# Optimization experiments

Measured on AMD Instinct MI355X. Metric: run time of the kernel, lower is better.

## Reference

```python
import jax, jax.numpy as jnp
import numpy as np


def _maxpool(x, k):
    # NCHW max pool with window k, stride k, no padding
    return jax.lax.reduce_window(
        x, -jnp.inf, jax.lax.max,
        window_dimensions=(1, 1, k, k),
        window_strides=(1, 1, k, k),
        padding='VALID')


def setup_inputs() -> dict:
    key = jax.random.key(0)
    k1, k2, k3, k4, k5 = jax.random.split(key, 5)
    return {
        'input_tensor1': jax.random.normal(k1, (8, 128, 56, 56), dtype=jnp.float32),
        'input_tensor2': jax.random.normal(k2, (8, 64, 112, 112), dtype=jnp.float32),
        'input_tensor3': jax.random.normal(k3, (8, 32, 224, 224), dtype=jnp.float32),
        'input_tensor4': jax.random.normal(k4, (8, 16, 448, 448), dtype=jnp.float32),
        'pure_ff': jax.random.normal(k5, (8, 256, 28, 28), dtype=jnp.float32),
    }


def reference(input_tensor1, input_tensor2, input_tensor3, input_tensor4, pure_ff):
    # Original: cat input k times along channels, then maxpool. Pooling is
    # channel-independent, so pool-once-then-tile is mathematically identical
    # (the cat pattern [x,x,...,x] is an exact channel tiling).
    x1 = jnp.tile(_maxpool(input_tensor1, 2), (1, 2, 1, 1))
    x2 = jnp.tile(_maxpool(input_tensor2, 4), (1, 4, 1, 1))
    x3 = jnp.tile(_maxpool(input_tensor3, 8), (1, 8, 1, 1))
    x4 = jnp.tile(_maxpool(input_tensor4, 16), (1, 16, 1, 1))
    return jax.nn.relu(x1 + x2 + x3 + x4 + pure_ff)
```

## Files before the change

kernel.cpp:

```cpp
#include <hip/hip_runtime.h>

#define DEVINL __device__ __forceinline__

DEVINL float fmax4(float4 v) { return fmaxf(fmaxf(v.x, v.y), fmaxf(v.z, v.w)); }
DEVINL float4 max44(float4 a, float4 b) {
    float4 r; r.x = fmaxf(a.x, b.x); r.y = fmaxf(a.y, b.y);
    r.z = fmaxf(a.z, b.z); r.w = fmaxf(a.w, b.w); return r;
}

#define MEMBAR() asm volatile("" ::: "memory")

#define O1 0
#define O2 802816
#define O3 1204224
#define O4 1404928
#define WS_FLOATS 1505280

#define W_T4 3584
#define W_T3 10752
#define W_T2 14336
#define W_T1 21504

__global__ __launch_bounds__(256, 4) void pool_all(
    const float* __restrict__ t1, const float* __restrict__ t2,
    const float* __restrict__ t3, const float* __restrict__ t4,
    float* __restrict__ ws)
{
    __shared__ __align__(16) float scratch[4 * 448];
    const int tid  = threadIdx.x;
    const int lane = tid & 63;
    const int w    = blockIdx.x * 4 + (tid >> 6);
    float* sm = &scratch[(tid >> 6) * 448];

    if (w < W_T4) {
        const int ph = w % 28, cb = w / 28;
        const float* base = t4 + (size_t)cb * 200704 + ph * 7168 + 4 * lane;
        float4 v[14], acc[7];
        #pragma unroll
        for (int k = 0; k < 7; ++k) v[k]     = *(const float4*)(base + k * 256);
        #pragma unroll
        for (int k = 0; k < 7; ++k) v[7 + k] = *(const float4*)(base + 1792 + k * 256);
        MEMBAR();
        #pragma unroll
        for (int k = 0; k < 7; ++k) acc[k] = max44(v[k], v[7 + k]);
        #pragma unroll
        for (int k = 0; k < 7; ++k) v[k]     = *(const float4*)(base + 3584 + k * 256);
        #pragma unroll
        for (int k = 0; k < 7; ++k) v[7 + k] = *(const float4*)(base + 5376 + k * 256);
        MEMBAR();
        #pragma unroll
        for (int k = 0; k < 7; ++k) acc[k] = max44(acc[k], max44(v[k], v[7 + k]));
        #pragma unroll
        for (int k = 0; k < 7; ++k) sm[k * 64 + lane] = fmax4(acc[k]);
        MEMBAR();
        if (lane < 28) {
            float4 a = *(const float4*)&sm[0 * 112 + 4 * lane];
            float4 b = *(const float4*)&sm[1 * 112 + 4 * lane];
            float4 c = *(const float4*)&sm[2 * 112 + 4 * lane];
            float4 d = *(const float4*)&sm[3 * 112 + 4 * lane];
            ws[O4 + cb * 784 + ph * 28 + lane] =
                fmax4(max44(max44(a, b), max44(c, d)));
        }
    } else if (w < W_T3) {
        const int t = w - W_T4;
        const int ph = t % 28, cb = t / 28;
        const float* base = t3 + (size_t)cb * 50176 + ph * 1792 + 4 * lane;
        float4 v[7];
        #pragma unroll
        for (int k = 0; k < 7; ++k) v[k] = *(const float4*)(base + k * 256);
        MEMBAR();
        #pragma unroll
        for (int k = 0; k < 7; ++k) sm[k * 64 + lane] = fmax4(v[k]);
        MEMBAR();
        if (lane < 28) {
            float m = fmaxf(sm[2 * lane], sm[2 * lane + 1]);
            #pragma unroll
            for (int r = 1; r < 8; ++r)
                m = fmaxf(m, fmaxf(sm[r * 56 + 2 * lane], sm[r * 56 + 2 * lane + 1]));
            ws[O3 + cb * 784 + ph * 28 + lane] = m;
        }
    } else if (w < W_T2) {
        const int t = w - W_T3;
        const int phq = t % 7, cb = t / 7;
        const float* base = t2 + (size_t)cb * 12544 + phq * 1792 + 4 * lane;
        float4 v[7];
        #pragma unroll
        for (int k = 0; k < 7; ++k) v[k] = *(const float4*)(base + k * 256);
        MEMBAR();
        #pragma unroll
        for (int k = 0; k < 7; ++k) sm[k * 64 + lane] = fmax4(v[k]);
        MEMBAR();
        if (lane < 56) {
            const int pr0 = lane / 28, pc = lane % 28;
            #pragma unroll
            for (int h = 0; h < 2; ++h) {
                const int pr = pr0 + 2 * h;
                float m = fmaxf(fmaxf(sm[(4 * pr + 0) * 28 + pc],
                                      sm[(4 * pr + 1) * 28 + pc]),
                                fmaxf(sm[(4 * pr + 2) * 28 + pc],
                                      sm[(4 * pr + 3) * 28 + pc]));
                ws[O2 + cb * 784 + phq * 112 + pr * 28 + pc] = m;
            }
        }
    } else {
        const int t = w - W_T2;
        const int phq = t % 7, cb = t / 7;
        const float* base = t1 + (size_t)cb * 3136 + phq * 448;
        if (lane < 56) {
            float4 a = *(const float4*)(base + 4 * lane);
            float4 b = *(const float4*)(base + 224 + 4 * lane);
            MEMBAR();
            float2 ha; ha.x = fmaxf(a.x, a.y); ha.y = fmaxf(a.z, a.w);
            float2 hb; hb.x = fmaxf(b.x, b.y); hb.y = fmaxf(b.z, b.w);
            const int ra = lane / 14, c2 = lane % 14;
            *(float2*)&sm[ra * 28 + 2 * c2]       = ha;
            *(float2*)&sm[(ra + 4) * 28 + 2 * c2] = hb;
        }
        MEMBAR();
        if (lane < 56) {
            const int pr0 = lane / 28, j = lane % 28;
            #pragma unroll
            for (int h = 0; h < 2; ++h) {
                const int pr = pr0 + 2 * h;
                float m = fmaxf(sm[(2 * pr) * 28 + j], sm[(2 * pr + 1) * 28 + j]);
                ws[O1 + cb * 784 + phq * 112 + pr * 28 + j] = m;
            }
        }
    }
}

__global__ __launch_bounds__(256) void combine(
    const float* __restrict__ ws, const float* __restrict__ ff,
    float* __restrict__ out)
{
    const int i4 = blockIdx.x * 256 + threadIdx.x;
    const int pw4 = i4 % 7;
    const int ph  = (i4 / 7) % 28;
    const int c   = (i4 / 196) % 256;
    const int b   = i4 / 50176;
    const int ppw = ph * 7 + pw4;
    const float4* W = (const float4*)ws;
    float4 a1 = W[O1 / 4 + (b * 128 + (c & 127)) * 196 + ppw];
    float4 a2 = W[O2 / 4 + (b * 64  + (c & 63))  * 196 + ppw];
    float4 a3 = W[O3 / 4 + (b * 32  + (c & 31))  * 196 + ppw];
    float4 a4 = W[O4 / 4 + (b * 16  + (c & 15))  * 196 + ppw];
    float4 f  = ((const float4*)ff)[i4];
    float4 o;
    o.x = fmaxf(a1.x + a2.x + a3.x + a4.x + f.x, 0.0f);
    o.y = fmaxf(a1.y + a2.y + a3.y + a4.y + f.y, 0.0f);
    o.z = fmaxf(a1.z + a2.z + a3.z + a4.z + f.z, 0.0f);
    o.w = fmaxf(a1.w + a2.w + a3.w + a4.w + f.w, 0.0f);
    ((float4*)out)[i4] = o;
}

__global__ __launch_bounds__(256) void fused_pool_relu(
    const float* __restrict__ t1, const float* __restrict__ t2,
    const float* __restrict__ t3, const float* __restrict__ t4,
    const float* __restrict__ ff, float* __restrict__ out)
{
    const int pwq = blockIdx.x, ph = blockIdx.y, b = blockIdx.z;
    const int tid = threadIdx.x;
    const int pw0 = pwq * 4;
    __shared__ __align__(16) float p1[128 * 4];
    __shared__ __align__(16) float p2[64 * 4];
    __shared__ __align__(16) float p3[32 * 4];
    __shared__ __align__(16) float p4[16 * 4];
    {
        const int g = tid >> 4, l = tid & 15;
        const float* base = t4 + ((size_t)(b * 16 + g) * 448 + ph * 16) * 448
                          + pw0 * 16 + l * 4;
        float4 v[8];
        #pragma unroll
        for (int r = 0; r < 8; ++r) v[r] = *(const float4*)(base + r * 448);
        float4 acc = v[0];
        #pragma unroll
        for (int r = 1; r < 8; ++r) acc = max44(acc, v[r]);
        #pragma unroll
        for (int r = 8; r < 16; ++r) v[r - 8] = *(const float4*)(base + r * 448);
        #pragma unroll
        for (int r = 0; r < 8; ++r) acc = max44(acc, v[r]);
        float m = fmax4(acc);
        m = fmaxf(m, __shfl_xor(m, 1));
        m = fmaxf(m, __shfl_xor(m, 2));
        if ((l & 3) == 0) p4[g * 4 + (l >> 2)] = m;
    }
    {
        const int g = tid >> 3, l = tid & 7;
        const float* base = t3 + ((size_t)(b * 32 + g) * 224 + ph * 8) * 224
                          + pw0 * 8 + l * 4;
        float4 v[8];
        #pragma unroll
        for (int r = 0; r < 8; ++r) v[r] = *(const float4*)(base + r * 224);
        float4 acc = v[0];
        #pragma unroll
        for (int r = 1; r < 8; ++r) acc = max44(acc, v[r]);
        float m = fmax4(acc);
        m = fmaxf(m, __shfl_xor(m, 1));
        if ((l & 1) == 0) p3[g * 4 + (l >> 1)] = m;
    }
    {
        const int g = tid >> 2, l = tid & 3;
        const float* base = t2 + ((size_t)(b * 64 + g) * 112 + ph * 4) * 112
                          + pw0 * 4 + l * 4;
        float4 v[4];
        #pragma unroll
        for (int r = 0; r < 4; ++r) v[r] = *(const float4*)(base + r * 112);
        p2[g * 4 + l] = fmax4(max44(max44(v[0], v[1]), max44(v[2], v[3])));
    }
    {
        const int g = tid >> 1, l = tid & 1;
        const float* base = t1 + ((size_t)(b * 128 + g) * 56 + ph * 2) * 56
                          + pw0 * 2 + l * 4;
        float4 a = max44(*(const float4*)(base), *(const float4*)(base + 56));
        p1[g * 4 + l * 2 + 0] = fmaxf(a.x, a.y);
        p1[g * 4 + l * 2 + 1] = fmaxf(a.z, a.w);
    }
    __syncthreads();
    const int c = tid;
    const int o4 = (b * 200704 + c * 784 + ph * 28 + pw0) >> 2;
    const float4 f  = ((const float4*)ff)[o4];
    const float4 a1 = *(const float4*)&p1[(c & 127) * 4];
    const float4 a2 = *(const float4*)&p2[(c & 63) * 4];
    const float4 a3 = *(const float4*)&p3[(c & 31) * 4];
    const float4 a4 = *(const float4*)&p4[(c & 15) * 4];
    float4 o;
    o.x = fmaxf(a1.x + a2.x + a3.x + a4.x + f.x, 0.0f);
    o.y = fmaxf(a1.y + a2.y + a3.y + a4.y + f.y, 0.0f);
    o.z = fmaxf(a1.z + a2.z + a3.z + a4.z + f.z, 0.0f);
    o.w = fmaxf(a1.w + a2.w + a3.w + a4.w + f.w, 0.0f);
    ((float4*)out)[o4] = o;
}

extern "C" void kernel_launch(void* const* d_in, const int* in_sizes, int n_in,
                              void* d_out, int out_size, void* d_ws, size_t ws_size,
                              hipStream_t stream) {
    const float* t1 = (const float*)d_in[0];
    const float* t2 = (const float*)d_in[1];
    const float* t3 = (const float*)d_in[2];
    const float* t4 = (const float*)d_in[3];
    const float* ff = (const float*)d_in[4];
    float* out = (float*)d_out;

    if (ws_size >= (size_t)WS_FLOATS * sizeof(float)) {
        float* ws = (float*)d_ws;
        pool_all<<<W_T1 / 4, 256, 0, stream>>>(t1, t2, t3, t4, ws);
        combine<<<1568, 256, 0, stream>>>(ws, ff, out);
    } else {
        dim3 grid(7, 28, 8);
        fused_pool_relu<<<grid, 256, 0, stream>>>(t1, t2, t3, t4, ff, out);
    }
}
```

Before: 225.3 us.

## Coarsen pooling waves to four tiles each with double-buffered register prefetch

Result: no change. 224.3 us (-0.4%).

```diff
diff --git a/kernel.cpp b/kernel.cpp
--- a/kernel.cpp
+++ b/kernel.cpp
@@ -16,40 +16,44 @@
 #define O4 1404928
 #define WS_FLOATS 1505280
 
-#define W_T4 3584
-#define W_T3 10752
-#define W_T2 14336
-#define W_T1 21504
+#define WE4 3584
+#define WE3 5376
+#define WE2 6272
+#define WE1 6720
+
+#define LD7(DST, PTR)                                                     \
+    { _Pragma("unroll") for (int k = 0; k < 7; ++k)                        \
+          DST[k] = *(const float4*)((PTR) + k * 256); }
 
 __global__ __launch_bounds__(256, 4) void pool_all(
     const float* __restrict__ t1, const float* __restrict__ t2,
     const float* __restrict__ t3, const float* __restrict__ t4,
     float* __restrict__ ws)
 {
-    __shared__ __align__(16) float scratch[4 * 448];
+    __shared__ __align__(16) float scratch[4 * 896];
     const int tid  = threadIdx.x;
     const int lane = tid & 63;
     const int w    = blockIdx.x * 4 + (tid >> 6);
-    float* sm = &scratch[(tid >> 6) * 448];
-
-    if (w < W_T4) {
-        const int ph = w % 28, cb = w / 28;
-        const float* base = t4 + (size_t)cb * 200704 + ph * 7168 + 4 * lane;
-        float4 v[14], acc[7];
-        #pragma unroll
-        for (int k = 0; k < 7; ++k) v[k]     = *(const float4*)(base + k * 256);
-        #pragma unroll
-        for (int k = 0; k < 7; ++k) v[7 + k] = *(const float4*)(base + 1792 + k * 256);
-        MEMBAR();
-        #pragma unroll
-        for (int k = 0; k < 7; ++k) acc[k] = max44(v[k], v[7 + k]);
-        #pragma unroll
-        for (int k = 0; k < 7; ++k) v[k]     = *(const float4*)(base + 3584 + k * 256);
-        #pragma unroll
-        for (int k = 0; k < 7; ++k) v[7 + k] = *(const float4*)(base + 5376 + k * 256);
-        MEMBAR();
-        #pragma unroll
-        for (int k = 0; k < 7; ++k) acc[k] = max44(acc[k], max44(v[k], v[7 + k]));
+    float* sm = &scratch[(tid >> 6) * 896];
+
+    if (w < WE4) {
+        const float* base = t4 + (size_t)w * 7168 + 4 * lane;
+        float4 A[7], B[7], acc[7];
+        LD7(A, base);
+        LD7(B, base + 1792);
+        MEMBAR();
+        #pragma unroll
+        for (int k = 0; k < 7; ++k) acc[k] = A[k];
+        LD7(A, base + 3584);
+        MEMBAR();
+        #pragma unroll
+        for (int k = 0; k < 7; ++k) acc[k] = max44(acc[k], B[k]);
+        LD7(B, base + 5376);
+        MEMBAR();
+        #pragma unroll
+        for (int k = 0; k < 7; ++k) acc[k] = max44(acc[k], A[k]);
+        #pragma unroll
+        for (int k = 0; k < 7; ++k) acc[k] = max44(acc[k], B[k]);
         #pragma unroll
         for (int k = 0; k < 7; ++k) sm[k * 64 + lane] = fmax4(acc[k]);
         MEMBAR();
@@ -58,74 +62,94 @@
             float4 b = *(const float4*)&sm[1 * 112 + 4 * lane];
             float4 c = *(const float4*)&sm[2 * 112 + 4 * lane];
             float4 d = *(const float4*)&sm[3 * 112 + 4 * lane];
-            ws[O4 + cb * 784 + ph * 28 + lane] =
-                fmax4(max44(max44(a, b), max44(c, d)));
-        }
-    } else if (w < W_T3) {
-        const int t = w - W_T4;
-        const int ph = t % 28, cb = t / 28;
-        const float* base = t3 + (size_t)cb * 50176 + ph * 1792 + 4 * lane;
-        float4 v[7];
-        #pragma unroll
-        for (int k = 0; k < 7; ++k) v[k] = *(const float4*)(base + k * 256);
-        MEMBAR();
-        #pragma unroll
-        for (int k = 0; k < 7; ++k) sm[k * 64 + lane] = fmax4(v[k]);
-        MEMBAR();
-        if (lane < 28) {
-            float m = fmaxf(sm[2 * lane], sm[2 * lane + 1]);
-            #pragma unroll
-            for (int r = 1; r < 8; ++r)
-                m = fmaxf(m, fmaxf(sm[r * 56 + 2 * lane], sm[r * 56 + 2 * lane + 1]));
-            ws[O3 + cb * 784 + ph * 28 + lane] = m;
-        }
-    } else if (w < W_T2) {
-        const int t = w - W_T3;
-        const int phq = t % 7, cb = t / 7;
-        const float* base = t2 + (size_t)cb * 12544 + phq * 1792 + 4 * lane;
-        float4 v[7];
-        #pragma unroll
-        for (int k = 0; k < 7; ++k) v[k] = *(const float4*)(base + k * 256);
-        MEMBAR();
-        #pragma unroll
-        for (int k = 0; k < 7; ++k) sm[k * 64 + lane] = fmax4(v[k]);
-        MEMBAR();
-        if (lane < 56) {
-            const int pr0 = lane / 28, pc = lane % 28;
-            #pragma unroll
-            for (int h = 0; h < 2; ++h) {
-                const int pr = pr0 + 2 * h;
-                float m = fmaxf(fmaxf(sm[(4 * pr + 0) * 28 + pc],
-                                      sm[(4 * pr + 1) * 28 + pc]),
-                                fmaxf(sm[(4 * pr + 2) * 28 + pc],
-                                      sm[(4 * pr + 3) * 28 + pc]));
-                ws[O2 + cb * 784 + phq * 112 + pr * 28 + pc] = m;
-            }
-        }
+            ws[O4 + w * 28 + lane] = fmax4(max44(max44(a, b), max44(c, d)));
+        }
+    } else if (w < WE3) {
+        const int t0 = (w - WE4) * 4;
+        const float* base = t3 + (size_t)t0 * 1792 + 4 * lane;
+        float4 A[7], B[7];
+        LD7(A, base);
+        LD7(B, base + 1792);
+        MEMBAR();
+        #define T3_UNIT(VV, i)                                                 \
+        {                                                                      \
+            float* smh = sm + ((i) & 1) * 448;                                 \
+            _Pragma("unroll") for (int k = 0; k < 7; ++k)                      \
+                smh[k * 64 + lane] = fmax4(VV[k]);          \
+            if ((i) + 2 < 4) LD7(VV, base + ((i) + 2) * 1792);                 \
+            MEMBAR();                                                          \
+            if (lane < 28) {                                                   \
+                float m = fmaxf(smh[2 * lane], smh[2 * lane + 1]);             \
+                _Pragma("unroll") for (int r = 1; r < 8; ++r)                  \
+                    m = fmaxf(m, fmaxf(smh[r * 56 + 2 * lane],                 \
+                                       smh[r * 56 + 2 * lane + 1]));           \
+                ws[O3 + (t0 + (i)) * 28 + lane] = m;                           \
+            }                                                                  \
+        }
+        T3_UNIT(A, 0)
+        T3_UNIT(B, 1)
+        T3_UNIT(A, 2)
+        T3_UNIT(B, 3)
+    } else if (w < WE2) {
+        const int t0 = (w - WE3) * 4;
+        const float* base = t2 + (size_t)t0 * 1792 + 4 * lane;
+        float4 A[7], B[7];
+        LD7(A, base);
+        LD7(B, base + 1792);
+        MEMBAR();
+        #define T2_UNIT(VV, i)                                                 \
+        {                                                                      \
+            float* smh = sm + ((i) & 1) * 448;                                 \
+            _Pragma("unroll") for (int k = 0; k < 7; ++k)                      \
+                smh[k * 64 + lane] = fmax4(VV[k]);                             \
+            if ((i) + 2 < 4) LD7(VV, base + ((i) + 2) * 1792);                 \
+            MEMBAR();                                                          \
+            if (lane < 56) {                                                   \
+                const int pr0 = lane / 28, pc = lane % 28;                     \
+                _Pragma("unroll") for (int h = 0; h < 2; ++h) {                \
+                    const int pr = pr0 + 2 * h;                                \
+                    float m = fmaxf(fmaxf(smh[(4 * pr + 0) * 28 + pc],         \
+                                          smh[(4 * pr + 1) * 28 + pc]),        \
+                                    fmaxf(smh[(4 * pr + 2) * 28 + pc],         \
+                                          smh[(4 * pr + 3) * 28 + pc]));       \
+                    ws[O2 + (t0 + (i)) * 112 + pr * 28 + pc] = m;              \
+                }                                                              \
+            }                                                                  \
+        }
+        T2_UNIT(A, 0)
+        T2_UNIT(B, 1)
+        T2_UNIT(A, 2)
+        T2_UNIT(B, 3)
     } else {
-        const int t = w - W_T2;
-        const int phq = t % 7, cb = t / 7;
-        const float* base = t1 + (size_t)cb * 3136 + phq * 448;
-        if (lane < 56) {
-            float4 a = *(const float4*)(base + 4 * lane);
-            float4 b = *(const float4*)(base + 224 + 4 * lane);
-            MEMBAR();
-            float2 ha; ha.x = fmaxf(a.x, a.y); ha.y = fmaxf(a.z, a.w);
-            float2 hb; hb.x = fmaxf(b.x, b.y); hb.y = fmaxf(b.z, b.w);
-            const int ra = lane / 14, c2 = lane % 14;
-            *(float2*)&sm[ra * 28 + 2 * c2]       = ha;
-            *(float2*)&sm[(ra + 4) * 28 + 2 * c2] = hb;
-        }
-        MEMBAR();
-        if (lane < 56) {
-            const int pr0 = lane / 28, j = lane % 28;
-            #pragma unroll
-            for (int h = 0; h < 2; ++h) {
-                const int pr = pr0 + 2 * h;
-                float m = fmaxf(sm[(2 * pr) * 28 + j], sm[(2 * pr + 1) * 28 + j]);
-                ws[O1 + cb * 784 + phq * 112 + pr * 28 + j] = m;
-            }
-        }
+        const int t0 = (w - WE2) * 4;
+        const float* base = t1 + (size_t)t0 * 1792 + 4 * lane;
+        float4 A[7], B[7];
+        LD7(A, base);
+        LD7(B, base + 1792);
+        MEMBAR();
+        #define T1_UNIT(VV, i)                                                 \
+        {                                                                      \
+            _Pragma("unroll") for (int k = 0; k < 7; ++k) {                    \
+                const int p = k * 64 + lane;                                   \
+                const int r = p / 14, c = p % 14;                              \
+                float2 h;                                                      \
+                h.x = fmaxf(VV[k].x, VV[k].y);                                 \
+                h.y = fmaxf(VV[k].z, VV[k].w);                                 \
+                *(float2*)&sm[r * 28 + 2 * c] = h;                             \
+            }                                                                  \
+            if ((i) + 2 < 4) LD7(VV, base + ((i) + 2) * 1792);                 \
+            MEMBAR();                                                          \
+            _Pragma("unroll") for (int h = 0; h < 7; ++h) {                    \
+                const int idx = h * 64 + lane;                                 \
+                const int q = idx / 28, j = idx % 28;                          \
+                ws[O1 + (t0 + (i)) * 448 + idx] =                              \
+                    fmaxf(sm[q * 56 + j], sm[q * 56 + j + 28]);                \
+            }                                                                  \
+        }
+        T1_UNIT(A, 0)
+        T1_UNIT(B, 1)
+        T1_UNIT(A, 2)
+        T1_UNIT(B, 3)
     }
 }
 
@@ -243,7 +267,7 @@
 
     if (ws_size >= (size_t)WS_FLOATS * sizeof(float)) {
         float* ws = (float*)d_ws;
-        pool_all<<<W_T1 / 4, 256, 0, stream>>>(t1, t2, t3, t4, ws);
+        pool_all<<<WE1 / 4, 256, 0, stream>>>(t1, t2, t3, t4, ws);
         combine<<<1568, 256, 0, stream>>>(ws, ff, out);
     } else {
         dim3 grid(7, 28, 8);
```

## Fuse all pooling levels and combine into one row-per-block kernel

Applied to the files above, without the earlier changes.

Result: no change. 225.2 us (-0.1%).

```diff
diff --git a/kernel.cpp b/kernel.cpp
--- a/kernel.cpp
+++ b/kernel.cpp
@@ -10,225 +10,173 @@
 
 #define MEMBAR() asm volatile("" ::: "memory")
 
-#define O1 0
-#define O2 802816
-#define O3 1204224
-#define O4 1404928
-#define WS_FLOATS 1505280
+#define P4O 0
+#define P3O 448
+#define P2O 1344
+#define P1O 3136
+#define SCRO 6720
+#define LDS_FLOATS 13888
 
-#define W_T4 3584
-#define W_T3 10752
-#define W_T2 14336
-#define W_T1 21504
+#define LD7(DST, PTR)                                                      \
+    { _Pragma("unroll") for (int k = 0; k < 7; ++k)                        \
+          DST[k] = *(const float4*)((PTR) + k * 256); }
 
-__global__ __launch_bounds__(256, 4) void pool_all(
-    const float* __restrict__ t1, const float* __restrict__ t2,
-    const float* __restrict__ t3, const float* __restrict__ t4,
-    float* __restrict__ ws)
-{
-    __shared__ __align__(16) float scratch[4 * 448];
-    const int tid  = threadIdx.x;
-    const int lane = tid & 63;
-    const int w    = blockIdx.x * 4 + (tid >> 6);
-    float* sm = &scratch[(tid >> 6) * 448];
+#define LD7T2(DST, EOFF)                                                   \
+    { _Pragma("unroll") for (int k = 0; k < 7; ++k) {                      \
+          const int f = k * 64 + lane;                                     \
+          DST[k] = *(const float4*)(base2 + (EOFF) + (f / 112) * 12544     \
+                                    + (f % 112) * 4); } }
 
-    if (w < W_T4) {
-        const int ph = w % 28, cb = w / 28;
-        const float* base = t4 + (size_t)cb * 200704 + ph * 7168 + 4 * lane;
-        float4 v[14], acc[7];
-        #pragma unroll
-        for (int k = 0; k < 7; ++k) v[k]     = *(const float4*)(base + k * 256);
-        #pragma unroll
-        for (int k = 0; k < 7; ++k) v[7 + k] = *(const float4*)(base + 1792 + k * 256);
-        MEMBAR();
-        #pragma unroll
-        for (int k = 0; k < 7; ++k) acc[k] = max44(v[k], v[7 + k]);
-        #pragma unroll
-        for (int k = 0; k < 7; ++k) v[k]     = *(const float4*)(base + 3584 + k * 256);
-        #pragma unroll
-        for (int k = 0; k < 7; ++k) v[7 + k] = *(const float4*)(base + 5376 + k * 256);
-        MEMBAR();
-        #pragma unroll
-        for (int k = 0; k < 7; ++k) acc[k] = max44(acc[k], max44(v[k], v[7 + k]));
-        #pragma unroll
-        for (int k = 0; k < 7; ++k) sm[k * 64 + lane] = fmax4(acc[k]);
-        MEMBAR();
-        if (lane < 28) {
-            float4 a = *(const float4*)&sm[0 * 112 + 4 * lane];
-            float4 b = *(const float4*)&sm[1 * 112 + 4 * lane];
-            float4 c = *(const float4*)&sm[2 * 112 + 4 * lane];
-            float4 d = *(const float4*)&sm[3 * 112 + 4 * lane];
-            ws[O4 + cb * 784 + ph * 28 + lane] =
-                fmax4(max44(max44(a, b), max44(c, d)));
-        }
-    } else if (w < W_T3) {
-        const int t = w - W_T4;
-        const int ph = t % 28, cb = t / 28;
-        const float* base = t3 + (size_t)cb * 50176 + ph * 1792 + 4 * lane;
-        float4 v[7];
-        #pragma unroll
-        for (int k = 0; k < 7; ++k) v[k] = *(const float4*)(base + k * 256);
-        MEMBAR();
-        #pragma unroll
-        for (int k = 0; k < 7; ++k) sm[k * 64 + lane] = fmax4(v[k]);
-        MEMBAR();
-        if (lane < 28) {
-            float m = fmaxf(sm[2 * lane], sm[2 * lane + 1]);
-            #pragma unroll
-            for (int r = 1; r < 8; ++r)
-                m = fmaxf(m, fmaxf(sm[r * 56 + 2 * lane], sm[r * 56 + 2 * lane + 1]));
-            ws[O3 + cb * 784 + ph * 28 + lane] = m;
-        }
-    } else if (w < W_T2) {
-        const int t = w - W_T3;
-        const int phq = t % 7, cb = t / 7;
-        const float* base = t2 + (size_t)cb * 12544 + phq * 1792 + 4 * lane;
-        float4 v[7];
-        #pragma unroll
-        for (int k = 0; k < 7; ++k) v[k] = *(const float4*)(base + k * 256);
-        MEMBAR();
-        #pragma unroll
-        for (int k = 0; k < 7; ++k) sm[k * 64 + lane] = fmax4(v[k]);
-        MEMBAR();
-        if (lane < 56) {
-            const int pr0 = lane / 28, pc = lane % 28;
-            #pragma unroll
-            for (int h = 0; h < 2; ++h) {
-                const int pr = pr0 + 2 * h;
-                float m = fmaxf(fmaxf(sm[(4 * pr + 0) * 28 + pc],
-                                      sm[(4 * pr + 1) * 28 + pc]),
-                                fmaxf(sm[(4 * pr + 2) * 28 + pc],
-                                      sm[(4 * pr + 3) * 28 + pc]));
-                ws[O2 + cb * 784 + phq * 112 + pr * 28 + pc] = m;
-            }
-        }
-    } else {
-        const int t = w - W_T2;
-        const int phq = t % 7, cb = t / 7;
-        const float* base = t1 + (size_t)cb * 3136 + phq * 448;
-        if (lane < 56) {
-            float4 a = *(const float4*)(base + 4 * lane);
-            float4 b = *(const float4*)(base + 224 + 4 * lane);
-            MEMBAR();
-            float2 ha; ha.x = fmaxf(a.x, a.y); ha.y = fmaxf(a.z, a.w);
-            float2 hb; hb.x = fmaxf(b.x, b.y); hb.y = fmaxf(b.z, b.w);
-            const int ra = lane / 14, c2 = lane % 14;
-            *(float2*)&sm[ra * 28 + 2 * c2]       = ha;
-            *(float2*)&sm[(ra + 4) * 28 + 2 * c2] = hb;
-        }
-        MEMBAR();
-        if (lane < 56) {
-            const int pr0 = lane / 28, j = lane % 28;
-            #pragma unroll
-            for (int h = 0; h < 2; ++h) {
-                const int pr = pr0 + 2 * h;
-                float m = fmaxf(sm[(2 * pr) * 28 + j], sm[(2 * pr + 1) * 28 + j]);
-                ws[O1 + cb * 784 + phq * 112 + pr * 28 + j] = m;
-            }
-        }
-    }
-}
+#define LD7T1(DST)                                                         \
+    { _Pragma("unroll") for (int k = 0; k < 7; ++k) {                      \
+          const int f = k * 64 + lane;                                     \
+          DST[k] = *(const float4*)(base1 + (f / 28) * 3136                \
+                                    + (f % 28) * 4); } }
 
-__global__ __launch_bounds__(256) void combine(
-    const float* __restrict__ ws, const float* __restrict__ ff,
-    float* __restrict__ out)
-{
-    const int i4 = blockIdx.x * 256 + threadIdx.x;
-    const int pw4 = i4 % 7;
-    const int ph  = (i4 / 7) % 28;
-    const int c   = (i4 / 196) % 256;
-    const int b   = i4 / 50176;
-    const int ppw = ph * 7 + pw4;
-    const float4* W = (const float4*)ws;
-    float4 a1 = W[O1 / 4 + (b * 128 + (c & 127)) * 196 + ppw];
-    float4 a2 = W[O2 / 4 + (b * 64  + (c & 63))  * 196 + ppw];
-    float4 a3 = W[O3 / 4 + (b * 32  + (c & 31))  * 196 + ppw];
-    float4 a4 = W[O4 / 4 + (b * 16  + (c & 15))  * 196 + ppw];
-    float4 f  = ((const float4*)ff)[i4];
-    float4 o;
-    o.x = fmaxf(a1.x + a2.x + a3.x + a4.x + f.x, 0.0f);
-    o.y = fmaxf(a1.y + a2.y + a3.y + a4.y + f.y, 0.0f);
-    o.z = fmaxf(a1.z + a2.z + a3.z + a4.z + f.z, 0.0f);
-    o.w = fmaxf(a1.w + a2.w + a3.w + a4.w + f.w, 0.0f);
-    ((float4*)out)[i4] = o;
-}
+#define ACCSET(V) { _Pragma("unroll") for (int k = 0; k < 7; ++k) acc[k] = V[k]; }
+#define ACCMAX(V) { _Pragma("unroll") for (int k = 0; k < 7; ++k) acc[k] = max44(acc[k], V[k]); }
 
-__global__ __launch_bounds__(256) void fused_pool_relu(
+#define GATH4(E)                                                           \
+    { _Pragma("unroll") for (int k = 0; k < 7; ++k)                        \
+          sm[k * 64 + lane] = fmax4(acc[k]);                               \
+      MEMBAR();                                                            \
+      if (lane < 28) {                                                     \
+          float4 ga = *(const float4*)&sm[0 * 112 + 4 * lane];             \
+          float4 gb = *(const float4*)&sm[1 * 112 + 4 * lane];             \
+          float4 gc = *(const float4*)&sm[2 * 112 + 4 * lane];             \
+          float4 gd = *(const float4*)&sm[3 * 112 + 4 * lane];             \
+          lds[P4O + (2 * ww + (E)) * 28 + lane] =                          \
+              fmax4(max44(max44(ga, gb), max44(gc, gd))); } }
+
+#define T3W(V, H)                                                          \
+    { float* smh = sm + (H) * 448;                                         \
+      _Pragma("unroll") for (int k = 0; k < 7; ++k)                        \
+          smh[k * 64 + lane] = fmax4(V[k]); }
+#define T3G(I, H)                                                          \
+    { float* smh = sm + (H) * 448;                                         \
+      if (lane < 28) {                                                     \
+          float2 p0 = *(const float2*)&smh[2 * lane];                      \
+          float m = fmaxf(p0.x, p0.y);                                     \
+          _Pragma("unroll") for (int r = 1; r < 8; ++r) {                  \
+              float2 pr = *(const float2*)&smh[r * 56 + 2 * lane];         \
+              m = fmaxf(m, fmaxf(pr.x, pr.y)); }                          \
+          lds[P3O + (4 * ww + (I)) * 28 + lane] = m; } }
+
+#define T2W(V, H)                                                          \
+    { float* smh = sm + (H) * 448;                                         \
+      _Pragma("unroll") for (int k = 0; k < 7; ++k)                        \
+          smh[k * 64 + lane] = fmax4(V[k]); }
+#define T2G(E, H)                                                          \
+    { float* smh = sm + (H) * 448;                                         \
+      if (lane < 56) {                                                     \
+          _Pragma("unroll") for (int h2 = 0; h2 < 2; ++h2) {               \
+              const int o = lane + 56 * h2;                                \
+              const int cc = o / 28, j = o % 28;                           \
+              float m = fmaxf(fmaxf(smh[cc * 112 + 0 * 28 + j],            \
+                                    smh[cc * 112 + 1 * 28 + j]),           \
+                              fmaxf(smh[cc * 112 + 2 * 28 + j],            \
+                                    smh[cc * 112 + 3 * 28 + j]));          \
+              lds[P2O + (8 * ww + 4 * (E) + cc) * 28 + j] = m; } } }
+
+#define T1W(V)                                                             \
+    { _Pragma("unroll") for (int k = 0; k < 7; ++k) {                      \
+          const int f = k * 64 + lane;                                     \
+          float2 hh; hh.x = fmaxf(V[k].x, V[k].y);                         \
+          hh.y = fmaxf(V[k].z, V[k].w);                                    \
+          *(float2*)&sm[2 * f] = hh; } }
+#define T1G()                                                              \
+    { _Pragma("unroll") for (int h2 = 0; h2 < 7; ++h2) {                   \
+          const int idx = h2 * 64 + lane;                                  \
+          const int cc = idx / 28, j = idx % 28;                           \
+          lds[P1O + (16 * ww + cc) * 28 + j] =                             \
+              fmaxf(sm[cc * 56 + j], sm[cc * 56 + 28 + j]); } }
+
+__global__ __launch_bounds__(512, 2) void fused_all(
     const float* __restrict__ t1, const float* __restrict__ t2,
     const float* __restrict__ t3, const float* __restrict__ t4,
     const float* __restrict__ ff, float* __restrict__ out)
 {
-    const int pwq = blockIdx.x, ph = blockIdx.y, b = blockIdx.z;
-    const int tid = threadIdx.x;
-    const int pw0 = pwq * 4;
-    __shared__ __align__(16) float p1[128 * 4];
-    __shared__ __align__(16) float p2[64 * 4];
-    __shared__ __align__(16) float p3[32 * 4];
-    __shared__ __align__(16) float p4[16 * 4];
-    {
-        const int g = tid >> 4, l = tid & 15;
-        const float* base = t4 + ((size_t)(b * 16 + g) * 448 + ph * 16) * 448
-                          + pw0 * 16 + l * 4;
-        float4 v[8];
-        #pragma unroll
-        for (int r = 0; r < 8; ++r) v[r] = *(const float4*)(base + r * 448);
-        float4 acc = v[0];
-        #pragma unroll
-        for (int r = 1; r < 8; ++r) acc = max44(acc, v[r]);
-        #pragma unroll
-        for (int r = 8; r < 16; ++r) v[r - 8] = *(const float4*)(base + r * 448);
-        #pragma unroll
-        for (int r = 0; r < 8; ++r) acc = max44(acc, v[r]);
-        float m = fmax4(acc);
-        m = fmaxf(m, __shfl_xor(m, 1));
-        m = fmaxf(m, __shfl_xor(m, 2));
-        if ((l & 3) == 0) p4[g * 4 + (l >> 2)] = m;
+    __shared__ __align__(16) float lds[LDS_FLOATS];
+    const int tid  = threadIdx.x;
+    const int lane = tid & 63;
+    const int ww   = tid >> 6;
+    const int ph   = blockIdx.x;
+    const int b    = blockIdx.y;
+    float* sm = &lds[SCRO + ww * 896];
+
+    const float4* FF = (const float4*)ff;
+    float4 ffr[4];
+    #pragma unroll
+    for (int m = 0; m < 3; ++m) {
+        const int i4 = tid + 512 * m;
+        ffr[m] = FF[(size_t)(b * 256 + i4 / 7) * 196 + ph * 7 + i4 % 7];
     }
-    {
-        const int g = tid >> 3, l = tid & 7;
-        const float* base = t3 + ((size_t)(b * 32 + g) * 224 + ph * 8) * 224
-                          + pw0 * 8 + l * 4;
-        float4 v[8];
-        #pragma unroll
-        for (int r = 0; r < 8; ++r) v[r] = *(const float4*)(base + r * 224);
-        float4 acc = v[0];
-        #pragma unroll
-        for (int r = 1; r < 8; ++r) acc = max44(acc, v[r]);
-        float m = fmax4(acc);
-        m = fmaxf(m, __shfl_xor(m, 1));
-        if ((l & 1) == 0) p3[g * 4 + (l >> 1)] = m;
+    if (tid < 256) {
+        const int i4 = tid + 1536;
+        ffr[3] = FF[(size_t)(b * 256 + i4 / 7) * 196 + ph * 7 + i4 % 7];
     }
-    {
-        const int g = tid >> 2, l = tid & 3;
-        const float* base = t2 + ((size_t)(b * 64 + g) * 112 + ph * 4) * 112
-                          + pw0 * 4 + l * 4;
-        float4 v[4];
-        #pragma unroll
-        for (int r = 0; r < 4; ++r) v[r] = *(const float4*)(base + r * 112);
-        p2[g * 4 + l] = fmax4(max44(max44(v[0], v[1]), max44(v[2], v[3])));
+
+    const float* a4 = t4 + (size_t)b * 3211264 + (2 * ww) * 200704
+                    + ph * 16 * 448 + 4 * lane;
+    const float* b4 = a4 + 200704;
+    const float* c3 = t3 + (size_t)b * 1605632 + (4 * ww) * 50176
+                    + ph * 8 * 224 + 4 * lane;
+    const float* base2 = t2 + (size_t)b * 802816 + (8 * ww) * 12544
+                       + ph * 448;
+    const float* base1 = t1 + (size_t)b * 401408 + (16 * ww) * 3136
+                       + ph * 112;
+
+    float4 A[7], B[7], acc[7];
+    LD7(A, a4);
+    LD7(B, a4 + 1792);
+    MEMBAR();
+    ACCSET(A);
+    LD7(A, a4 + 3584); MEMBAR();
+    ACCMAX(B);
+    LD7(B, a4 + 5376); MEMBAR();
+    ACCMAX(A);
+    LD7(A, b4); MEMBAR();
+    ACCMAX(B);
+    LD7(B, b4 + 1792); MEMBAR();
+    GATH4(0);
+    ACCSET(A);
+    LD7(A, b4 + 3584); MEMBAR();
+    ACCMAX(B);
+    LD7(B, b4 + 5376); MEMBAR();
+    ACCMAX(A);
+    LD7(A, c3); MEMBAR();
+    ACCMAX(B);
+    LD7(B, c3 + 50176); MEMBAR();
+    GATH4(1);
+    T3W(A, 0); LD7(A, c3 + 2 * 50176); MEMBAR(); T3G(0, 0);
+    T3W(B, 1); LD7(B, c3 + 3 * 50176); MEMBAR(); T3G(1, 1);
+    T3W(A, 0); LD7T2(A, 0);            MEMBAR(); T3G(2, 0);
+    T3W(B, 1); LD7T2(B, 50176);        MEMBAR(); T3G(3, 1);
+    T2W(A, 0); LD7T1(A);               MEMBAR(); T2G(0, 0);
+    T2W(B, 1);                         MEMBAR(); T2G(1, 1);
+    T1W(A); MEMBAR(); T1G();
+
+    __syncthreads();
+
+    float4* O = (float4*)out;
+    #pragma unroll
+    for (int m = 0; m < 4; ++m) {
+        if (m < 3 || tid < 256) {
+            const int i4 = tid + 512 * m;
+            const int ch = i4 / 7, j4 = i4 % 7;
+            const float4 x1 = *(const float4*)&lds[P1O + (ch & 127) * 28 + 4 * j4];
+            const float4 x2 = *(const float4*)&lds[P2O + (ch & 63)  * 28 + 4 * j4];
+            const float4 x3 = *(const float4*)&lds[P3O + (ch & 31)  * 28 + 4 * j4];
+            const float4 x4 = *(const float4*)&lds[P4O + (ch & 15)  * 28 + 4 * j4];
+            const float4 f  = ffr[m];
+            float4 o;
+            o.x = fmaxf(x1.x + x2.x + x3.x + x4.x + f.x, 0.0f);
+            o.y = fmaxf(x1.y + x2.y + x3.y + x4.y + f.y, 0.0f);
+            o.z = fmaxf(x1.z + x2.z + x3.z + x4.z + f.z, 0.0f);
+            o.w = fmaxf(x1.w + x2.w + x3.w + x4.w + f.w, 0.0f);
+            O[(size_t)(b * 256 + ch) * 196 + ph * 7 + j4] = o;
+        }
     }
-    {
-        const int g = tid >> 1, l = tid & 1;
-        const float* base = t1 + ((size_t)(b * 128 + g) * 56 + ph * 2) * 56
-                          + pw0 * 2 + l * 4;
-        float4 a = max44(*(const float4*)(base), *(const float4*)(base + 56));
-        p1[g * 4 + l * 2 + 0] = fmaxf(a.x, a.y);
-        p1[g * 4 + l * 2 + 1] = fmaxf(a.z, a.w);
-    }
-    __syncthreads();
-    const int c = tid;
-    const int o4 = (b * 200704 + c * 784 + ph * 28 + pw0) >> 2;
-    const float4 f  = ((const float4*)ff)[o4];
-    const float4 a1 = *(const float4*)&p1[(c & 127) * 4];
-    const float4 a2 = *(const float4*)&p2[(c & 63) * 4];
-    const float4 a3 = *(const float4*)&p3[(c & 31) * 4];
-    const float4 a4 = *(const float4*)&p4[(c & 15) * 4];
-    float4 o;
-    o.x = fmaxf(a1.x + a2.x + a3.x + a4.x + f.x, 0.0f);
-    o.y = fmaxf(a1.y + a2.y + a3.y + a4.y + f.y, 0.0f);
-    o.z = fmaxf(a1.z + a2.z + a3.z + a4.z + f.z, 0.0f);
-    o.w = fmaxf(a1.w + a2.w + a3.w + a4.w + f.w, 0.0f);
-    ((float4*)out)[o4] = o;
 }
 
 extern "C" void kernel_launch(void* const* d_in, const int* in_sizes, int n_in,
@@ -239,14 +187,6 @@
     const float* t3 = (const float*)d_in[2];
     const float* t4 = (const float*)d_in[3];
     const float* ff = (const float*)d_in[4];
-    float* out = (float*)d_out;
-
-    if (ws_size >= (size_t)WS_FLOATS * sizeof(float)) {
-        float* ws = (float*)d_ws;
-        pool_all<<<W_T1 / 4, 256, 0, stream>>>(t1, t2, t3, t4, ws);
-        combine<<<1568, 256, 0, stream>>>(ws, ff, out);
-    } else {
-        dim3 grid(7, 28, 8);
-        fused_pool_relu<<<grid, 256, 0, stream>>>(t1, t2, t3, t4, ff, out);
-    }
+    dim3 grid(28, 8);
+    fused_all<<<grid, 512, 0, stream>>>(t1, t2, t3, t4, ff, (float*)d_out);
 }
```
